# Kernel tuning notes

Measured on AMD Instinct MI355X. Metric: run time of the kernel, lower is better.

The kernel has to match this reference:

```python
import jax, jax.numpy as jnp
import numpy as np

B, N, C = 8, 4096, 1024
ATT_DIM = 512
M = 64  # num_outputs


def setup_inputs() -> dict:
    key = jax.random.key(0)
    k_x, k_w, k_b, k_av = jax.random.split(key, 4)
    x = jax.random.normal(k_x, (B, N, C), dtype=jnp.float32)
    # nn.Linear(input_dim, attention_dim): weight (att, C), bias (att,)
    lim = 1.0 / np.sqrt(C)
    W = jax.random.uniform(k_w, (ATT_DIM, C), dtype=jnp.float32, minval=-lim, maxval=lim)
    b = jax.random.uniform(k_b, (ATT_DIM,), dtype=jnp.float32, minval=-lim, maxval=lim)
    # torch.rand -> uniform [0,1)
    attention_vectors = jax.random.uniform(k_av, (M, ATT_DIM), dtype=jnp.float32)
    return {"x": x, "W": W, "b": b, "attention_vectors": attention_vectors}


def reference(x, W, b, attention_vectors):
    # linear projection: (B,N,C) @ (C,att) + bias -> (B,N,att)
    scores = jnp.einsum('bnc,dc->bnd', x, W) + b
    # learned-query attention logits: (B,M,N)
    logits = jnp.einsum('bnd,md->bmn', scores, attention_vectors)
    weights = jax.nn.softmax(logits, axis=-1)
    # pool original features: (B,M,N) @ (B,N,C) -> (B,M,C)
    return jnp.einsum('bmn,bnc->bmc', weights, x)
```

## Files before the change

### kernel.cpp

```cpp
#include <hip/hip_runtime.h>
#include <hip/hip_bf16.h>

#define Bn 8
#define Nn 4096
#define Cn 1024
#define Dn 512
#define Mn 64

typedef __hip_bfloat16 bf16;
typedef __attribute__((ext_vector_type(8))) short short8;
typedef __attribute__((ext_vector_type(4))) short short4x;
typedef __attribute__((ext_vector_type(4))) float f32x4;

#define MFMA16(a, b, c) __builtin_amdgcn_mfma_f32_16x16x32_bf16((a), (b), (c), 0, 0, 0)

__device__ inline short bfbits(float f) {
  union { bf16 b; short s; } u;
  u.b = __float2bfloat16(f);
  return u.s;
}

__global__ __launch_bounds__(256) void prep_kernel(
    const float* __restrict__ W, const float* __restrict__ bias,
    const float* __restrict__ av, bf16* __restrict__ Vhi,
    bf16* __restrict__ Vlo, float* __restrict__ c0) {
  const int m = blockIdx.x;
  const int t = threadIdx.x;
  const int cl = t & 63, dg = t >> 6;
  const int c = blockIdx.y * 64 + cl;
  const float* wp = W + (size_t)(dg * 128) * Cn + c;
  const float* ap = av + m * Dn + dg * 128;
  float a0 = 0.f, a1 = 0.f, a2 = 0.f, a3 = 0.f;
#pragma unroll 8
  for (int i = 0; i < 128; i += 4) {
    a0 = fmaf(ap[i + 0], wp[(size_t)(i + 0) * Cn], a0);
    a1 = fmaf(ap[i + 1], wp[(size_t)(i + 1) * Cn], a1);
    a2 = fmaf(ap[i + 2], wp[(size_t)(i + 2) * Cn], a2);
    a3 = fmaf(ap[i + 3], wp[(size_t)(i + 3) * Cn], a3);
  }
  __shared__ float red[256];
  red[t] = (a0 + a1) + (a2 + a3);
  __syncthreads();
  const float v = red[cl] + red[cl + 64] + red[cl + 128] + red[cl + 192];
  if (dg == 0) {
    const bf16 hi = __float2bfloat16(v);
    Vhi[m * Cn + c] = hi;
    Vlo[m * Cn + c] = __float2bfloat16(v - __bfloat162float(hi));
  }
  if (blockIdx.y == 0) {
    __syncthreads();
    red[t] = av[m * Dn + t] * bias[t] + av[m * Dn + t + 256] * bias[t + 256];
    __syncthreads();
    if (t < 64) {
      float s = red[t] + red[t + 64] + red[t + 128] + red[t + 192];
#pragma unroll
      for (int off = 32; off > 0; off >>= 1) s += __shfl_down(s, off);
      if (t == 0) c0[m] = s;
    }
  }
}

__global__ __launch_bounds__(256) void logits_kernel(
    const float* __restrict__ x, const bf16* __restrict__ Vhi,
    const bf16* __restrict__ Vlo, const float* __restrict__ c0,
    float* __restrict__ logits) {
  const int n0 = blockIdx.x * 64;
  const int b = blockIdx.y;
  const int t = threadIdx.x;
  __shared__ short Xs[64][136];
  __shared__ short VsH[64][136];
  __shared__ short VsL[64][136];
  const int w = t >> 6, lane = t & 63, lr = lane & 15, q = lane >> 4;
  const ptrdiff_t dlo = Vlo - Vhi;

  int ur[4], uc[4];
  const float* xsrc[4];
  const bf16* hsrc[4];
#pragma unroll
  for (int j = 0; j < 4; ++j) {
    const int u = t + 256 * j;
    ur[j] = u >> 4;
    uc[j] = (u & 15) * 8;
    xsrc[j] = x + (size_t)(b * Nn + n0 + ur[j]) * Cn + uc[j];
    hsrc[j] = Vhi + ur[j] * Cn + uc[j];
  }

  f32x4 acc[4];
#pragma unroll
  for (int i = 0; i < 4; ++i) acc[i] = (f32x4){0.f, 0.f, 0.f, 0.f};

  float4 px0[4], px1[4];
  short8 pvh[4], pvl[4];
#pragma unroll
  for (int j = 0; j < 4; ++j) {
    px0[j] = *(const float4*)(xsrc[j]);
    px1[j] = *(const float4*)(xsrc[j] + 4);
    pvh[j] = *(const short8*)(hsrc[j]);
    pvl[j] = *(const short8*)(hsrc[j] + dlo);
  }

  for (int k0 = 0; k0 < Cn; k0 += 128) {
#pragma unroll
    for (int j = 0; j < 4; ++j) {
      short8 s;
      s[0] = bfbits(px0[j].x); s[1] = bfbits(px0[j].y);
      s[2] = bfbits(px0[j].z); s[3] = bfbits(px0[j].w);
      s[4] = bfbits(px1[j].x); s[5] = bfbits(px1[j].y);
      s[6] = bfbits(px1[j].z); s[7] = bfbits(px1[j].w);
      *(short8*)&Xs[ur[j]][uc[j]] = s;
      *(short8*)&VsH[ur[j]][uc[j]] = pvh[j];
      *(short8*)&VsL[ur[j]][uc[j]] = pvl[j];
    }
    __syncthreads();
    if (k0 + 128 < Cn) {
#pragma unroll
      for (int j = 0; j < 4; ++j) {
        px0[j] = *(const float4*)(xsrc[j] + k0 + 128);
        px1[j] = *(const float4*)(xsrc[j] + k0 + 132);
        pvh[j] = *(const short8*)(hsrc[j] + k0 + 128);
        pvl[j] = *(const short8*)(hsrc[j] + dlo + k0 + 128);
      }
    }
#pragma unroll
    for (int kk = 0; kk < 128; kk += 32) {
      const short8 a = *(const short8*)&Xs[w * 16 + lr][kk + q * 8];
#pragma unroll
      for (int mt = 0; mt < 4; ++mt) {
        acc[mt] = MFMA16(a, *(const short8*)&VsH[mt * 16 + lr][kk + q * 8], acc[mt]);
        acc[mt] = MFMA16(a, *(const short8*)&VsL[mt * 16 + lr][kk + q * 8], acc[mt]);
      }
    }
    __syncthreads();
  }
#pragma unroll
  for (int mt = 0; mt < 4; ++mt) {
    const int m = mt * 16 + lr;
    const float bb = c0[m];
    float4 o;
    o.x = acc[mt][0] + bb; o.y = acc[mt][1] + bb;
    o.z = acc[mt][2] + bb; o.w = acc[mt][3] + bb;
    *(float4*)&logits[(size_t)(b * Mn + m) * Nn + n0 + w * 16 + q * 4] = o;
  }
}

__global__ __launch_bounds__(256) void softmax_kernel(
    const float* __restrict__ logits, bf16* __restrict__ wgt) {
  const int row = blockIdx.x;
  const int t = threadIdx.x;
  const float* L = logits + (size_t)row * Nn;
  float v[16];
  float mx = -3.4e38f;
#pragma unroll
  for (int i = 0; i < 16; ++i) {
    v[i] = L[t + 256 * i];
    mx = fmaxf(mx, v[i]);
  }
#pragma unroll
  for (int off = 32; off > 0; off >>= 1) mx = fmaxf(mx, __shfl_down(mx, off));
  __shared__ float sred[4];
  if ((t & 63) == 0) sred[t >> 6] = mx;
  __syncthreads();
  mx = fmaxf(fmaxf(sred[0], sred[1]), fmaxf(sred[2], sred[3]));
  float sum = 0.f;
#pragma unroll
  for (int i = 0; i < 16; ++i) {
    v[i] = __expf(v[i] - mx);
    sum += v[i];
  }
#pragma unroll
  for (int off = 32; off > 0; off >>= 1) sum += __shfl_down(sum, off);
  __syncthreads();
  if ((t & 63) == 0) sred[t >> 6] = sum;
  __syncthreads();
  const float inv = 1.f / (sred[0] + sred[1] + sred[2] + sred[3]);
#pragma unroll
  for (int i = 0; i < 16; ++i)
    wgt[(size_t)row * Nn + t + 256 * i] = __float2bfloat16(v[i] * inv);
}

__global__ __launch_bounds__(256) void pool_kernel(
    const float* __restrict__ x, const bf16* __restrict__ wgt,
    float* __restrict__ part) {
  const int cbase = blockIdx.x * 64;
  const int b = blockIdx.y;
  const int ks = blockIdx.z;
  const int t = threadIdx.x;
  __shared__ short XT[64][136];
  const int w = t >> 6, lane = t & 63, lr = lane & 15, q = lane >> 4;
  const int mh = (w & 1) * 32, ch = (w >> 1) * 32;
  f32x4 acc[2][2];
#pragma unroll
  for (int i = 0; i < 2; ++i)
#pragma unroll
    for (int j = 0; j < 2; ++j) acc[i][j] = (f32x4){0.f, 0.f, 0.f, 0.f};

  const int h = t & 15, g = t >> 4;
  const int swz = 8 * (h & 7);
  const int swzr0 = 8 * (((ch + lr) >> 2) & 7);
  const int swzr1 = 8 * (((ch + 16 + lr) >> 2) & 7);
  const int kbase = ks * (Nn / 4);
  const float* xsrc = x + (size_t)b * Nn * Cn + (size_t)(kbase + 4 * g) * Cn + cbase + 4 * h;
  const bf16* wr0 = wgt + (size_t)(b * Mn + mh + lr) * Nn + kbase;
  const bf16* wr1 = wr0 + (size_t)16 * Nn;

  float4 pf[8];
#pragma unroll
  for (int i = 0; i < 4; ++i) {
    pf[i]     = *(const float4*)(xsrc + (size_t)i * Cn);
    pf[4 + i] = *(const float4*)(xsrc + (size_t)(64 + i) * Cn);
  }

  for (int kc = 0; kc < Nn / 4; kc += 128) {
#pragma unroll
    for (int blk = 0; blk < 2; ++blk) {
      const float4 r0 = pf[blk * 4 + 0], r1 = pf[blk * 4 + 1];
      const float4 r2 = pf[blk * 4 + 2], r3 = pf[blk * 4 + 3];
      const int kof = (blk * 64 + 4 * g) ^ swz;
      short4x v0, v1, v2, v3;
      v0[0] = bfbits(r0.x); v0[1] = bfbits(r1.x); v0[2] = bfbits(r2.x); v0[3] = bfbits(r3.x);
      v1[0] = bfbits(r0.y); v1[1] = bfbits(r1.y); v1[2] = bfbits(r2.y); v1[3] = bfbits(r3.y);
      v2[0] = bfbits(r0.z); v2[1] = bfbits(r1.z); v2[2] = bfbits(r2.z); v2[3] = bfbits(r3.z);
      v3[0] = bfbits(r0.w); v3[1] = bfbits(r1.w); v3[2] = bfbits(r2.w); v3[3] = bfbits(r3.w);
      *(short4x*)&XT[4 * h + 0][kof] = v0;
      *(short4x*)&XT[4 * h + 1][kof] = v1;
      *(short4x*)&XT[4 * h + 2][kof] = v2;
      *(short4x*)&XT[4 * h + 3][kof] = v3;
    }
    __syncthreads();
    if (kc + 128 < Nn / 4) {
#pragma unroll
      for (int i = 0; i < 4; ++i) {
        pf[i]     = *(const float4*)(xsrc + (size_t)(kc + 128 + i) * Cn);
        pf[4 + i] = *(const float4*)(xsrc + (size_t)(kc + 192 + i) * Cn);
      }
    }
#pragma unroll
    for (int kk = 0; kk < 128; kk += 32) {
      const short8 a0 = *(const short8*)(wr0 + kc + kk + q * 8);
      const short8 a1 = *(const short8*)(wr1 + kc + kk + q * 8);
      const short8 b0 = *(const short8*)&XT[ch + lr][(kk + q * 8) ^ swzr0];
      const short8 b1 = *(const short8*)&XT[ch + 16 + lr][(kk + q * 8) ^ swzr1];
      acc[0][0] = MFMA16(a0, b0, acc[0][0]);
      acc[0][1] = MFMA16(a0, b1, acc[0][1]);
      acc[1][0] = MFMA16(a1, b0, acc[1][0]);
      acc[1][1] = MFMA16(a1, b1, acc[1][1]);
    }
    __syncthreads();
  }
  float* pout = part + ((size_t)ks * Bn + b) * Mn * Cn;
#pragma unroll
  for (int mi = 0; mi < 2; ++mi)
#pragma unroll
    for (int ci = 0; ci < 2; ++ci) {
      const int m = mh + mi * 16 + q * 4;
      const int c = cbase + ch + ci * 16 + lr;
#pragma unroll
      for (int reg = 0; reg < 4; ++reg)
        pout[(size_t)(m + reg) * Cn + c] = acc[mi][ci][reg];
    }
}

__global__ __launch_bounds__(256) void reduce_kernel(
    const float* __restrict__ part, float* __restrict__ out) {
  const int i = blockIdx.x * 256 + threadIdx.x;
  const float4* p = (const float4*)part;
  const int S4 = (Bn * Mn * Cn) / 4;
  const float4 v0 = p[i], v1 = p[i + S4], v2 = p[i + 2 * S4], v3 = p[i + 3 * S4];
  float4 o;
  o.x = (v0.x + v1.x) + (v2.x + v3.x);
  o.y = (v0.y + v1.y) + (v2.y + v3.y);
  o.z = (v0.z + v1.z) + (v2.z + v3.z);
  o.w = (v0.w + v1.w) + (v2.w + v3.w);
  ((float4*)out)[i] = o;
}

extern "C" void kernel_launch(void* const* d_in, const int* in_sizes, int n_in,
                              void* d_out, int out_size, void* d_ws, size_t ws_size,
                              hipStream_t stream) {
  const float* x = (const float*)d_in[0];
  const float* W = (const float*)d_in[1];
  const float* bias = (const float*)d_in[2];
  const float* av = (const float*)d_in[3];
  float* out = (float*)d_out;
  char* ws = (char*)d_ws;

  bf16* Vhi = (bf16*)(ws + 0);
  bf16* Vlo = (bf16*)(ws + 131072);
  float* c0 = (float*)(ws + 262144);
  float* logits = (float*)(ws + 263168);
  bf16* wgt = (bf16*)(ws + 8651776);
  float* part = (float*)(ws + 12846080);

  prep_kernel<<<dim3(Mn, Cn / 64), 256, 0, stream>>>(W, bias, av, Vhi, Vlo, c0);
  logits_kernel<<<dim3(Nn / 64, Bn), 256, 0, stream>>>(x, Vhi, Vlo, c0, logits);
  softmax_kernel<<<Bn * Mn, 256, 0, stream>>>(logits, wgt);
  pool_kernel<<<dim3(Cn / 64, Bn, 4), 256, 0, stream>>>(x, wgt, part);
  reduce_kernel<<<(Bn * Mn * Cn) / 1024, 256, 0, stream>>>(part, out);
}
```

Measured before the change: 244.7 us.

## Double-buffer LDS in logits and pool kernels, load x directly to registers

The logits kernel now reads x straight from global memory into MFMA A-operand registers instead of staging it through shared memory. It double-buffers only the V hi/lo tiles in 64-wide k chunks and stages its output through LDS so the logits stores are coalesced. The pool kernel moves to a double-buffered 64-wide XT tile with one barrier per step, and prefetches the weight fragments into registers one step ahead. The aim is to overlap global loads with MFMA work and cut LDS footprint and barriers, at the cost of more registers and less coalesced direct x reads.

```diff
diff --git a/kernel.cpp b/kernel.cpp
--- a/kernel.cpp
+++ b/kernel.cpp
@@ -18,6 +18,13 @@
   union { bf16 b; short s; } u;
   u.b = __float2bfloat16(f);
   return u.s;
+}
+
+__device__ inline short8 pack8(const float4& a, const float4& b) {
+  short8 s;
+  s[0] = bfbits(a.x); s[1] = bfbits(a.y); s[2] = bfbits(a.z); s[3] = bfbits(a.w);
+  s[4] = bfbits(b.x); s[5] = bfbits(b.y); s[6] = bfbits(b.z); s[7] = bfbits(b.w);
+  return s;
 }
 
 __global__ __launch_bounds__(256) void prep_kernel(
@@ -67,79 +74,105 @@
   const int n0 = blockIdx.x * 64;
   const int b = blockIdx.y;
   const int t = threadIdx.x;
-  __shared__ short Xs[64][136];
-  __shared__ short VsH[64][136];
-  __shared__ short VsL[64][136];
+  __shared__ short Vs[2][2][64][72];
   const int w = t >> 6, lane = t & 63, lr = lane & 15, q = lane >> 4;
-  const ptrdiff_t dlo = Vlo - Vhi;
-
-  int ur[4], uc[4];
-  const float* xsrc[4];
-  const bf16* hsrc[4];
-#pragma unroll
-  for (int j = 0; j < 4; ++j) {
+
+  int vr[2], vc[2];
+  const bf16 *hsrc[2], *lsrc[2];
+#pragma unroll
+  for (int j = 0; j < 2; ++j) {
     const int u = t + 256 * j;
-    ur[j] = u >> 4;
-    uc[j] = (u & 15) * 8;
-    xsrc[j] = x + (size_t)(b * Nn + n0 + ur[j]) * Cn + uc[j];
-    hsrc[j] = Vhi + ur[j] * Cn + uc[j];
-  }
+    vr[j] = u >> 3;
+    vc[j] = (u & 7) * 8;
+    hsrc[j] = Vhi + vr[j] * Cn + vc[j];
+    lsrc[j] = Vlo + vr[j] * Cn + vc[j];
+  }
+  const float* xrow = x + (size_t)(b * Nn + n0 + w * 16 + lr) * Cn + q * 8;
 
   f32x4 acc[4];
 #pragma unroll
   for (int i = 0; i < 4; ++i) acc[i] = (f32x4){0.f, 0.f, 0.f, 0.f};
 
-  float4 px0[4], px1[4];
-  short8 pvh[4], pvl[4];
-#pragma unroll
-  for (int j = 0; j < 4; ++j) {
-    px0[j] = *(const float4*)(xsrc[j]);
-    px1[j] = *(const float4*)(xsrc[j] + 4);
-    pvh[j] = *(const short8*)(hsrc[j]);
-    pvl[j] = *(const short8*)(hsrc[j] + dlo);
-  }
-
-  for (int k0 = 0; k0 < Cn; k0 += 128) {
-#pragma unroll
-    for (int j = 0; j < 4; ++j) {
-      short8 s;
-      s[0] = bfbits(px0[j].x); s[1] = bfbits(px0[j].y);
-      s[2] = bfbits(px0[j].z); s[3] = bfbits(px0[j].w);
-      s[4] = bfbits(px1[j].x); s[5] = bfbits(px1[j].y);
-      s[6] = bfbits(px1[j].z); s[7] = bfbits(px1[j].w);
-      *(short8*)&Xs[ur[j]][uc[j]] = s;
-      *(short8*)&VsH[ur[j]][uc[j]] = pvh[j];
-      *(short8*)&VsL[ur[j]][uc[j]] = pvl[j];
+  short8 vh[2], vl[2];
+  float4 xs0, xs1, xs2, xs3;
+
+#pragma unroll
+  for (int j = 0; j < 2; ++j) {
+    vh[j] = *(const short8*)(hsrc[j]);
+    vl[j] = *(const short8*)(lsrc[j]);
+  }
+  xs0 = *(const float4*)(xrow);
+  xs1 = *(const float4*)(xrow + 4);
+  xs2 = *(const float4*)(xrow + 32);
+  xs3 = *(const float4*)(xrow + 36);
+#pragma unroll
+  for (int j = 0; j < 2; ++j) {
+    *(short8*)&Vs[0][0][vr[j]][vc[j]] = vh[j];
+    *(short8*)&Vs[0][1][vr[j]][vc[j]] = vl[j];
+  }
+#pragma unroll
+  for (int j = 0; j < 2; ++j) {
+    vh[j] = *(const short8*)(hsrc[j] + 64);
+    vl[j] = *(const short8*)(lsrc[j] + 64);
+  }
+  __syncthreads();
+
+#pragma unroll
+  for (int kc = 0; kc < 16; ++kc) {
+    const int buf = kc & 1;
+    const short8 a0 = pack8(xs0, xs1);
+    const short8 a1 = pack8(xs2, xs3);
+    if (kc < 15) {
+      const int k1 = (kc + 1) * 64;
+      xs0 = *(const float4*)(xrow + k1);
+      xs1 = *(const float4*)(xrow + k1 + 4);
+      xs2 = *(const float4*)(xrow + k1 + 32);
+      xs3 = *(const float4*)(xrow + k1 + 36);
+    }
+    if (kc < 15) {
+#pragma unroll
+      for (int j = 0; j < 2; ++j) {
+        *(short8*)&Vs[buf ^ 1][0][vr[j]][vc[j]] = vh[j];
+        *(short8*)&Vs[buf ^ 1][1][vr[j]][vc[j]] = vl[j];
+      }
+    }
+    if (kc < 14) {
+      const int k2 = (kc + 2) * 64;
+#pragma unroll
+      for (int j = 0; j < 2; ++j) {
+        vh[j] = *(const short8*)(hsrc[j] + k2);
+        vl[j] = *(const short8*)(lsrc[j] + k2);
+      }
+    }
+#pragma unroll
+    for (int kk2 = 0; kk2 < 2; ++kk2) {
+      const short8 a = kk2 ? a1 : a0;
+      const int ko = kk2 * 32 + q * 8;
+#pragma unroll
+      for (int mt = 0; mt < 4; ++mt) {
+        acc[mt] = MFMA16(a, *(const short8*)&Vs[buf][0][mt * 16 + lr][ko], acc[mt]);
+        acc[mt] = MFMA16(a, *(const short8*)&Vs[buf][1][mt * 16 + lr][ko], acc[mt]);
+      }
     }
     __syncthreads();
-    if (k0 + 128 < Cn) {
-#pragma unroll
-      for (int j = 0; j < 4; ++j) {
-        px0[j] = *(const float4*)(xsrc[j] + k0 + 128);
-        px1[j] = *(const float4*)(xsrc[j] + k0 + 132);
-        pvh[j] = *(const short8*)(hsrc[j] + k0 + 128);
-        pvl[j] = *(const short8*)(hsrc[j] + dlo + k0 + 128);
-      }
-    }
-#pragma unroll
-    for (int kk = 0; kk < 128; kk += 32) {
-      const short8 a = *(const short8*)&Xs[w * 16 + lr][kk + q * 8];
-#pragma unroll
-      for (int mt = 0; mt < 4; ++mt) {
-        acc[mt] = MFMA16(a, *(const short8*)&VsH[mt * 16 + lr][kk + q * 8], acc[mt]);
-        acc[mt] = MFMA16(a, *(const short8*)&VsL[mt * 16 + lr][kk + q * 8], acc[mt]);
-      }
-    }
-    __syncthreads();
-  }
+  }
+
+  float (*LT)[68] = reinterpret_cast<float(*)[68]>(&Vs[0][0][0][0]);
 #pragma unroll
   for (int mt = 0; mt < 4; ++mt) {
     const int m = mt * 16 + lr;
     const float bb = c0[m];
-    float4 o;
-    o.x = acc[mt][0] + bb; o.y = acc[mt][1] + bb;
-    o.z = acc[mt][2] + bb; o.w = acc[mt][3] + bb;
-    *(float4*)&logits[(size_t)(b * Mn + m) * Nn + n0 + w * 16 + q * 4] = o;
+    f32x4 o = acc[mt];
+    o[0] += bb; o[1] += bb; o[2] += bb; o[3] += bb;
+    *(f32x4*)&LT[m][w * 16 + q * 4] = o;
+  }
+  __syncthreads();
+  {
+    const int mr = t >> 2, seg = (t & 3) * 16;
+    const float* srcL = &LT[mr][seg];
+    float* dst = logits + (size_t)(b * Mn + mr) * Nn + n0 + seg;
+#pragma unroll
+    for (int i = 0; i < 4; ++i) *(float4*)(dst + 4 * i) = *(const float4*)(srcL + 4 * i);
   }
 }
 
@@ -185,7 +218,7 @@
   const int b = blockIdx.y;
   const int ks = blockIdx.z;
   const int t = threadIdx.x;
-  __shared__ short XT[64][136];
+  __shared__ short XT[2][64][72];
   const int w = t >> 6, lane = t & 63, lr = lane & 15, q = lane >> 4;
   const int mh = (w & 1) * 32, ch = (w >> 1) * 32;
   f32x4 acc[2][2];
@@ -200,53 +233,83 @@
   const int swzr1 = 8 * (((ch + 16 + lr) >> 2) & 7);
   const int kbase = ks * (Nn / 4);
   const float* xsrc = x + (size_t)b * Nn * Cn + (size_t)(kbase + 4 * g) * Cn + cbase + 4 * h;
-  const bf16* wr0 = wgt + (size_t)(b * Mn + mh + lr) * Nn + kbase;
+  const bf16* wr0 = wgt + (size_t)(b * Mn + mh + lr) * Nn + kbase + q * 8;
   const bf16* wr1 = wr0 + (size_t)16 * Nn;
 
-  float4 pf[8];
-#pragma unroll
-  for (int i = 0; i < 4; ++i) {
-    pf[i]     = *(const float4*)(xsrc + (size_t)i * Cn);
-    pf[4 + i] = *(const float4*)(xsrc + (size_t)(64 + i) * Cn);
-  }
-
-  for (int kc = 0; kc < Nn / 4; kc += 128) {
-#pragma unroll
-    for (int blk = 0; blk < 2; ++blk) {
-      const float4 r0 = pf[blk * 4 + 0], r1 = pf[blk * 4 + 1];
-      const float4 r2 = pf[blk * 4 + 2], r3 = pf[blk * 4 + 3];
-      const int kof = (blk * 64 + 4 * g) ^ swz;
+  float4 p0, p1, p2, p3;
+  short8 aw0, aw1, aw2, aw3;
+
+  p0 = *(const float4*)(xsrc);
+  p1 = *(const float4*)(xsrc + Cn);
+  p2 = *(const float4*)(xsrc + 2 * Cn);
+  p3 = *(const float4*)(xsrc + 3 * Cn);
+  aw0 = *(const short8*)(wr0);
+  aw1 = *(const short8*)(wr0 + 32);
+  aw2 = *(const short8*)(wr1);
+  aw3 = *(const short8*)(wr1 + 32);
+  {
+    const int kof = (4 * g) ^ swz;
+    short4x v0, v1, v2, v3;
+    v0[0] = bfbits(p0.x); v0[1] = bfbits(p1.x); v0[2] = bfbits(p2.x); v0[3] = bfbits(p3.x);
+    v1[0] = bfbits(p0.y); v1[1] = bfbits(p1.y); v1[2] = bfbits(p2.y); v1[3] = bfbits(p3.y);
+    v2[0] = bfbits(p0.z); v2[1] = bfbits(p1.z); v2[2] = bfbits(p2.z); v2[3] = bfbits(p3.z);
+    v3[0] = bfbits(p0.w); v3[1] = bfbits(p1.w); v3[2] = bfbits(p2.w); v3[3] = bfbits(p3.w);
+    *(short4x*)&XT[0][4 * h + 0][kof] = v0;
+    *(short4x*)&XT[0][4 * h + 1][kof] = v1;
+    *(short4x*)&XT[0][4 * h + 2][kof] = v2;
+    *(short4x*)&XT[0][4 * h + 3][kof] = v3;
+  }
+  p0 = *(const float4*)(xsrc + (size_t)64 * Cn);
+  p1 = *(const float4*)(xsrc + (size_t)65 * Cn);
+  p2 = *(const float4*)(xsrc + (size_t)66 * Cn);
+  p3 = *(const float4*)(xsrc + (size_t)67 * Cn);
+  __syncthreads();
+
+#pragma unroll 4
+  for (int kc = 0; kc < 16; ++kc) {
+    const int buf = kc & 1;
+    const short8 a00 = aw0, a01 = aw1, a10 = aw2, a11 = aw3;
+    if (kc < 15) {
+      const int k1 = (kc + 1) * 64;
+      aw0 = *(const short8*)(wr0 + k1);
+      aw1 = *(const short8*)(wr0 + k1 + 32);
+      aw2 = *(const short8*)(wr1 + k1);
+      aw3 = *(const short8*)(wr1 + k1 + 32);
+    }
+    if (kc < 15) {
+      const int kof = (4 * g) ^ swz;
       short4x v0, v1, v2, v3;
-      v0[0] = bfbits(r0.x); v0[1] = bfbits(r1.x); v0[2] = bfbits(r2.x); v0[3] = bfbits(r3.x);
-      v1[0] = bfbits(r0.y); v1[1] = bfbits(r1.y); v1[2] = bfbits(r2.y); v1[3] = bfbits(r3.y);
-      v2[0] = bfbits(r0.z); v2[1] = bfbits(r1.z); v2[2] = bfbits(r2.z); v2[3] = bfbits(r3.z);
-      v3[0] = bfbits(r0.w); v3[1] = bfbits(r1.w); v3[2] = bfbits(r2.w); v3[3] = bfbits(r3.w);
-      *(short4x*)&XT[4 * h + 0][kof] = v0;
-      *(short4x*)&XT[4 * h + 1][kof] = v1;
-      *(short4x*)&XT[4 * h + 2][kof] = v2;
-      *(short4x*)&XT[4 * h + 3][kof] = v3;
+      v0[0] = bfbits(p0.x); v0[1] = bfbits(p1.x); v0[2] = bfbits(p2.x); v0[3] = bfbits(p3.x);
+      v1[0] = bfbits(p0.y); v1[1] = bfbits(p1.y); v1[2] = bfbits(p2.y); v1[3] = bfbits(p3.y);
+      v2[0] = bfbits(p0.z); v2[1] = bfbits(p1.z); v2[2] = bfbits(p2.z); v2[3] = bfbits(p3.z);
+      v3[0] = bfbits(p0.w); v3[1] = bfbits(p1.w); v3[2] = bfbits(p2.w); v3[3] = bfbits(p3.w);
+      *(short4x*)&XT[buf ^ 1][4 * h + 0][kof] = v0;
+      *(short4x*)&XT[buf ^ 1][4 * h + 1][kof] = v1;
+      *(short4x*)&XT[buf ^ 1][4 * h + 2][kof] = v2;
+      *(short4x*)&XT[buf ^ 1][4 * h + 3][kof] = v3;
+    }
+    if (kc < 14) {
+      const size_t roff = (size_t)(kc + 2) * 64 * Cn;
+      p0 = *(const float4*)(xsrc + roff);
+      p1 = *(const float4*)(xsrc + roff + Cn);
+      p2 = *(const float4*)(xsrc + roff + 2 * Cn);
+      p3 = *(const float4*)(xsrc + roff + 3 * Cn);
+    }
+#pragma unroll
+    for (int kk2 = 0; kk2 < 2; ++kk2) {
+      const int ko = kk2 * 32 + q * 8;
+      const short8 b0 = *(const short8*)&XT[buf][ch + lr][ko ^ swzr0];
+      const short8 b1 = *(const short8*)&XT[buf][ch + 16 + lr][ko ^ swzr1];
+      const short8 aa = kk2 ? a01 : a00;
+      const short8 ab = kk2 ? a11 : a10;
+      acc[0][0] = MFMA16(aa, b0, acc[0][0]);
+      acc[0][1] = MFMA16(aa, b1, acc[0][1]);
+      acc[1][0] = MFMA16(ab, b0, acc[1][0]);
+      acc[1][1] = MFMA16(ab, b1, acc[1][1]);
     }
     __syncthreads();
-    if (kc + 128 < Nn / 4) {
-#pragma unroll
-      for (int i = 0; i < 4; ++i) {
-        pf[i]     = *(const float4*)(xsrc + (size_t)(kc + 128 + i) * Cn);
-        pf[4 + i] = *(const float4*)(xsrc + (size_t)(kc + 192 + i) * Cn);
-      }
-    }
-#pragma unroll
-    for (int kk = 0; kk < 128; kk += 32) {
-      const short8 a0 = *(const short8*)(wr0 + kc + kk + q * 8);
-      const short8 a1 = *(const short8*)(wr1 + kc + kk + q * 8);
-      const short8 b0 = *(const short8*)&XT[ch + lr][(kk + q * 8) ^ swzr0];
-      const short8 b1 = *(const short8*)&XT[ch + 16 + lr][(kk + q * 8) ^ swzr1];
-      acc[0][0] = MFMA16(a0, b0, acc[0][0]);
-      acc[0][1] = MFMA16(a0, b1, acc[0][1]);
-      acc[1][0] = MFMA16(a1, b0, acc[1][0]);
-      acc[1][1] = MFMA16(a1, b1, acc[1][1]);
-    }
-    __syncthreads();
-  }
+  }
+
   float* pout = part + ((size_t)ks * Bn + b) * Mn * Cn;
 #pragma unroll
   for (int mi = 0; mi < 2; ++mi)
```

After: 253.8 us. 1.04x slower.
